# Kernel optimization log

Measured on AMD Instinct MI355X. Metric: run time of the kernel, lower is better.

## Reference

```python
import jax, jax.numpy as jnp
import numpy as np

DIM = 1024
NUM_HEADS = 16
HEAD_DIM = DIM // NUM_HEADS
B, L = 2, 2048


def setup_inputs() -> dict:
    key = jax.random.key(0)
    k_x, k_qkv, k_pw, k_pb = jax.random.split(key, 4)
    x = jax.random.normal(k_x, (B, L, DIM), dtype=jnp.float32)
    # nn.Linear(dim, 3*dim, bias=False): weight [3*dim, dim]; y = x @ W.T
    w_qkv = jax.random.normal(k_qkv, (3 * DIM, DIM), dtype=jnp.float32) * (DIM ** -0.5)
    # nn.Linear(dim, dim) with bias
    w_proj = jax.random.normal(k_pw, (DIM, DIM), dtype=jnp.float32) * (DIM ** -0.5)
    b_proj = jax.random.normal(k_pb, (DIM,), dtype=jnp.float32) * 0.01
    return {"x": x, "w_qkv": w_qkv, "w_proj": w_proj, "b_proj": b_proj}


def reference(x, w_qkv, w_proj, b_proj):
    Bx, Lx, C = x.shape
    qkv = x @ w_qkv.T  # [B, L, 3C]
    qkv = qkv.reshape(Bx, Lx, 3, NUM_HEADS, HEAD_DIM)
    q = jnp.transpose(qkv[:, :, 0], (0, 2, 1, 3))  # [B, H, L, D]
    k = jnp.transpose(qkv[:, :, 1], (0, 2, 1, 3))
    v = jnp.transpose(qkv[:, :, 2], (0, 2, 1, 3))
    attn = jnp.einsum('bhqd,bhkd->bhqk', q, k) * (HEAD_DIM ** -0.5)
    attn = jax.nn.softmax(attn, axis=-1)
    out = jnp.einsum('bhqk,bhkd->bhqd', attn, v)  # [B, H, L, D]
    out = jnp.transpose(out, (0, 2, 1, 3)).reshape(Bx, Lx, C)
    return out @ w_proj.T + b_proj
```

## Files before the change

### kernel.cpp

```cpp
#include <hip/hip_runtime.h>

#define DIM 1024
#define NH 16
#define HD 64
#define BB 2
#define LL 2048
#define BL (BB*LL)
#define NQKV (3*DIM)

typedef __bf16 bf16;
typedef __bf16 bf16x4 __attribute__((ext_vector_type(4)));
typedef __bf16 bf16x8 __attribute__((ext_vector_type(8)));
typedef float  f32x4  __attribute__((ext_vector_type(4)));

#define QSCALE 0.1803368801111204f

typedef __attribute__((address_space(3))) unsigned int lds_u32;
typedef __attribute__((address_space(1))) unsigned int glb_u32;

__device__ __forceinline__ void gld_lds16(const bf16* g, bf16* l) {
    __builtin_amdgcn_global_load_lds((const glb_u32*)g, (lds_u32*)l, 16, 0, 0);
}

#define C0 (BL*DIM/4)
#define C1 (NQKV*DIM/4)
#define C2 (DIM*DIM/4)
__global__ __launch_bounds__(256) void cvt_all(const float* __restrict__ x,
        const float* __restrict__ wq, const float* __restrict__ wp,
        bf16* __restrict__ xb, bf16* __restrict__ wqb, bf16* __restrict__ wpb) {
    int i = blockIdx.x * 256 + threadIdx.x;
    const float* in; bf16* out; int j;
    if (i < C0)            { in = x;  out = xb;  j = i; }
    else if (i < C0 + C1)  { in = wq; out = wqb; j = i - C0; }
    else                   { in = wp; out = wpb; j = i - C0 - C1; }
    float4 f = ((const float4*)in)[j];
    bf16x4 o = { (bf16)f.x, (bf16)f.y, (bf16)f.z, (bf16)f.w };
    ((bf16x4*)out)[j] = o;
}

__global__ __launch_bounds__(256, 3) void gemm_qkv(
        const bf16* __restrict__ A, const bf16* __restrict__ W,
        bf16* __restrict__ Qb, bf16* __restrict__ Kb, bf16* __restrict__ VTb) {
    __shared__ bf16 As[128][64];
    __shared__ bf16 Bs[128][64];
    const int tid = threadIdx.x;
    const int w = tid >> 6, lane = tid & 63, quad = lane >> 4, l16 = lane & 15;
    const int n0 = blockIdx.x * 128, m0 = blockIdx.y * 128;
    const int wm = (w & 1) * 64, wn = (w >> 1) * 64;
    f32x4 acc[4][4] = {};
    for (int k0 = 0; k0 < DIM; k0 += 64) {
        #pragma unroll
        for (int i = 0; i < 4; ++i) {
            int cb = w * 256 + i * 64;
            int gc = cb + lane;
            int r = gc >> 3;
            int cs = (gc & 7) ^ (r & 7);
            gld_lds16(A + (size_t)(m0 + r) * DIM + k0 + cs*8, &As[0][0] + cb * 8);
            gld_lds16(W + (size_t)(n0 + r) * DIM + k0 + cs*8, &Bs[0][0] + cb * 8);
        }
        __syncthreads();
        #pragma unroll
        for (int kc = 0; kc < 2; ++kc) {
            bf16x8 af[4], bfr[4];
            #pragma unroll
            for (int t = 0; t < 4; ++t) {
                int rw = wn + t*16 + l16;
                int cw = (kc*4 + quad) ^ (rw & 7);
                af[t] = *(const bf16x8*)(&Bs[0][0] + rw*64 + cw*8);
                int rx = wm + t*16 + l16;
                int cx = (kc*4 + quad) ^ (rx & 7);
                bfr[t] = *(const bf16x8*)(&As[0][0] + rx*64 + cx*8);
            }
            #pragma unroll
            for (int tm = 0; tm < 4; ++tm)
                #pragma unroll
                for (int tn = 0; tn < 4; ++tn)
                    acc[tm][tn] = __builtin_amdgcn_mfma_f32_16x16x32_bf16(
                                      af[tm], bfr[tn], acc[tm][tn], 0, 0, 0);
        }
        __syncthreads();
    }
    const int which = n0 >> 10;
    #pragma unroll
    for (int tm = 0; tm < 4; ++tm) {
        int nb = n0 + wn + tm*16 + quad*4;
        int rem = nb & 1023, h = rem >> 6, db = rem & 63;
        #pragma unroll
        for (int tn = 0; tn < 4; ++tn) {
            int m = m0 + wm + tn*16 + l16;
            int b = m >> 11, l = m & 2047, bh = (b << 4) | h;
            if (which == 0) {
                bf16x4 q4 = { (bf16)(acc[tm][tn][0] * QSCALE),
                              (bf16)(acc[tm][tn][1] * QSCALE),
                              (bf16)(acc[tm][tn][2] * QSCALE),
                              (bf16)(acc[tm][tn][3] * QSCALE) };
                *(bf16x4*)(Qb + ((size_t)bh << 17) + ((size_t)l << 6) + db) = q4;
            } else if (which == 1) {
                bf16x4 k4 = { (bf16)acc[tm][tn][0], (bf16)acc[tm][tn][1],
                              (bf16)acc[tm][tn][2], (bf16)acc[tm][tn][3] };
                *(bf16x4*)(Kb + ((size_t)bh << 17) + ((size_t)l << 6) + db) = k4;
            } else {
                #pragma unroll
                for (int r = 0; r < 4; ++r)
                    VTb[((size_t)bh << 17) + ((size_t)(db + r) << 11) + l] =
                        (bf16)acc[tm][tn][r];
            }
        }
    }
}

__global__ __launch_bounds__(256, 3) void gemm_proj(
        const bf16* __restrict__ A, const bf16* __restrict__ W,
        const float* __restrict__ bias, float* __restrict__ out) {
    __shared__ bf16 As[128][64];
    __shared__ bf16 Bs[64][64];
    const int tid = threadIdx.x;
    const int w = tid >> 6, lane = tid & 63, quad = lane >> 4, l16 = lane & 15;
    const int n0 = blockIdx.x * 64, m0 = blockIdx.y * 128;
    const int wm = (w & 1) * 64, wn = (w >> 1) * 32;
    f32x4 acc[2][4] = {};
    for (int k0 = 0; k0 < DIM; k0 += 64) {
        #pragma unroll
        for (int i = 0; i < 4; ++i) {
            int cb = w * 256 + i * 64;
            int gc = cb + lane;
            int r = gc >> 3;
            int cs = (gc & 7) ^ (r & 7);
            gld_lds16(A + (size_t)(m0 + r) * DIM + k0 + cs*8, &As[0][0] + cb * 8);
        }
        #pragma unroll
        for (int i = 0; i < 2; ++i) {
            int cb = w * 128 + i * 64;
            int gc = cb + lane;
            int r = gc >> 3;
            int cs = (gc & 7) ^ (r & 7);
            gld_lds16(W + (size_t)(n0 + r) * DIM + k0 + cs*8, &Bs[0][0] + cb * 8);
        }
        __syncthreads();
        #pragma unroll
        for (int kc = 0; kc < 2; ++kc) {
            bf16x8 af[2], bfr[4];
            #pragma unroll
            for (int t = 0; t < 2; ++t) {
                int rw = wn + t*16 + l16;
                int cw = (kc*4 + quad) ^ (rw & 7);
                af[t] = *(const bf16x8*)(&Bs[0][0] + rw*64 + cw*8);
            }
            #pragma unroll
            for (int t = 0; t < 4; ++t) {
                int rx = wm + t*16 + l16;
                int cx = (kc*4 + quad) ^ (rx & 7);
                bfr[t] = *(const bf16x8*)(&As[0][0] + rx*64 + cx*8);
            }
            #pragma unroll
            for (int tm = 0; tm < 2; ++tm)
                #pragma unroll
                for (int tn = 0; tn < 4; ++tn)
                    acc[tm][tn] = __builtin_amdgcn_mfma_f32_16x16x32_bf16(
                                      af[tm], bfr[tn], acc[tm][tn], 0, 0, 0);
        }
        __syncthreads();
    }
    #pragma unroll
    for (int tm = 0; tm < 2; ++tm) {
        int nb = n0 + wn + tm*16 + quad*4;
        float4 b4 = *(const float4*)&bias[nb];
        #pragma unroll
        for (int tn = 0; tn < 4; ++tn) {
            int m = m0 + wm + tn*16 + l16;
            float4 o4 = { acc[tm][tn][0] + b4.x, acc[tm][tn][1] + b4.y,
                          acc[tm][tn][2] + b4.z, acc[tm][tn][3] + b4.w };
            *(float4*)(out + (size_t)m * DIM + nb) = o4;
        }
    }
}

__global__ __launch_bounds__(256, 2) void attn(
        const bf16* __restrict__ Qb, const bf16* __restrict__ Kb,
        const bf16* __restrict__ VTb, bf16* __restrict__ AO) {
    __shared__ bf16 Ks[2][64][64];
    __shared__ bf16 VTs[2][64][64];
    const int tid = threadIdx.x;
    const int w = tid >> 6, lane = tid & 63, quad = lane >> 4, l16 = lane & 15;
    const int qt = blockIdx.x, bh = blockIdx.y;
    const bf16* Qg = Qb + ((size_t)bh << 17) + (size_t)(qt * 128) * 64;
    const bf16* Kg = Kb + ((size_t)bh << 17);
    const bf16* Vg = VTb + ((size_t)bh << 17);

    bf16x8 aq[2][2];
    #pragma unroll
    for (int sub = 0; sub < 2; ++sub)
        #pragma unroll
        for (int kd = 0; kd < 2; ++kd)
            aq[sub][kd] = *(const bf16x8*)(Qg + (size_t)(w*32 + sub*16 + l16) * 64
                                           + kd*32 + quad*8);

    bf16x8 onesf = {};
    if (l16 == 0)
        #pragma unroll
        for (int j = 0; j < 8; ++j) onesf[j] = (bf16)1.0f;

    f32x4 oacc[2][4] = {};
    f32x4 lacc[2] = {};
    bf16x8 apA[2][2], apB[2][2];

    auto stageK = [&](int kt, int buf) {
        #pragma unroll
        for (int i = 0; i < 2; ++i) {
            int gc = w*128 + i*64 + lane;
            int r = gc >> 3;
            int cs = (gc & 7) ^ (r & 7) ^ ((r >> 3) & 7) ^ ((r & 1) << 2);
            gld_lds16(Kg + (size_t)(kt*64 + r) * 64 + cs*8,
                      &Ks[buf][0][0] + gc * 8);
        }
    };
    auto stageV = [&](int kt, int buf) {
        #pragma unroll
        for (int i = 0; i < 2; ++i) {
            int gc = w*128 + i*64 + lane;
            int r = gc >> 3;
            int cs = (gc & 7) ^ (r & 7) ^ ((r >> 3) & 7);
            gld_lds16(Vg + (size_t)r * 2048 + kt*64 + cs*8,
                      &VTs[buf][0][0] + gc * 8);
        }
    };
    auto pv = [&](int pbuf, bf16x8 (&ap)[2][2]) {
        #pragma unroll
        for (int kk = 0; kk < 2; ++kk) {
            #pragma unroll
            for (int nt = 0; nt < 4; ++nt) {
                int row = nt*16 + l16;
                int cp = (kk*4 + quad) ^ (row & 7) ^ ((row >> 3) & 7);
                bf16x8 bv = *(const bf16x8*)(&VTs[pbuf][0][0] + row*64 + cp*8);
                #pragma unroll
                for (int sub = 0; sub < 2; ++sub)
                    oacc[sub][nt] = __builtin_amdgcn_mfma_f32_16x16x32_bf16(
                                        ap[sub][kk], bv, oacc[sub][nt], 0, 0, 0);
            }
            #pragma unroll
            for (int sub = 0; sub < 2; ++sub)
                lacc[sub] = __builtin_amdgcn_mfma_f32_16x16x32_bf16(
                                ap[sub][kk], onesf, lacc[sub], 0, 0, 0);
        }
    };

    auto body = [&](int kt, int cur, bf16x8 (&apw)[2][2], bf16x8 (&apr)[2][2]) {
        __syncthreads();
        if (kt < 31) stageK(kt + 1, cur ^ 1);
        stageV(kt, cur);

        f32x4 s[2][2][2] = {};
        #pragma unroll
        for (int kk = 0; kk < 2; ++kk)
            #pragma unroll
            for (int u = 0; u < 2; ++u)
                #pragma unroll
                for (int kd = 0; kd < 2; ++kd) {
                    int rk = kk*32 + ((l16 >> 2) << 3) + u*4 + (l16 & 3);
                    int cs = (kd*4 + quad) ^ (rk & 7) ^ ((rk >> 3) & 7)
                             ^ ((rk & 1) << 2);
                    bf16x8 ak = *(const bf16x8*)(&Ks[cur][0][0] + rk*64 + cs*8);
                    #pragma unroll
                    for (int sub = 0; sub < 2; ++sub)
                        s[sub][kk][u] = __builtin_amdgcn_mfma_f32_16x16x32_bf16(
                                            ak, aq[sub][kd], s[sub][kk][u], 0, 0, 0);
                }

        if (kt > 0) pv(cur ^ 1, apr);

        #pragma unroll
        for (int sub = 0; sub < 2; ++sub)
            #pragma unroll
            for (int kk = 0; kk < 2; ++kk) {
                bf16x8 p;
                #pragma unroll
                for (int u = 0; u < 2; ++u)
                    #pragma unroll
                    for (int r = 0; r < 4; ++r)
                        p[u*4 + r] = (bf16)exp2f(s[sub][kk][u][r]);
                apw[sub][kk] = p;
            }
    };

    stageK(0, 0);
    for (int kt2 = 0; kt2 < 32; kt2 += 2) {
        body(kt2,     0, apA, apB);
        body(kt2 + 1, 1, apB, apA);
    }
    __syncthreads();
    pv(1, apB);

    const int b = bh >> 4, h = bh & 15;
    #pragma unroll
    for (int sub = 0; sub < 2; ++sub)
        #pragma unroll
        for (int r = 0; r < 4; ++r) {
            float l = __shfl(lacc[sub][r], quad * 16, 64);
            float inv = 1.0f / l;
            int lq = qt*128 + w*32 + sub*16 + quad*4 + r;
            size_t rowbase = ((size_t)(b * 2048 + lq)) * DIM + h * 64;
            #pragma unroll
            for (int nt = 0; nt < 4; ++nt)
                AO[rowbase + nt*16 + l16] = (bf16)(oacc[sub][nt][r] * inv);
        }
}

extern "C" void kernel_launch(void* const* d_in, const int* in_sizes, int n_in,
                              void* d_out, int out_size, void* d_ws, size_t ws_size,
                              hipStream_t stream) {
    const float* x      = (const float*)d_in[0];
    const float* w_qkv  = (const float*)d_in[1];
    const float* w_proj = (const float*)d_in[2];
    const float* b_proj = (const float*)d_in[3];
    float* out = (float*)d_out;
    char* ws = (char*)d_ws;

    bf16* xb  = (bf16*)(ws);
    bf16* wqb = (bf16*)(ws + ( 8u << 20));
    bf16* wpb = (bf16*)(ws + (14u << 20));
    bf16* Qb  = (bf16*)(ws + (16u << 20));
    bf16* Kb  = (bf16*)(ws + (24u << 20));
    bf16* VTb = (bf16*)(ws + (32u << 20));
    bf16* AOb = (bf16*)(ws + (40u << 20));

    cvt_all<<<(C0 + C1 + C2) / 256, 256, 0, stream>>>(x, w_qkv, w_proj, xb, wqb, wpb);
    gemm_qkv<<<dim3(NQKV/128, BL/128), 256, 0, stream>>>(xb, wqb, Qb, Kb, VTb);
    attn<<<dim3(LL/128, BB*NH),        256, 0, stream>>>(Qb, Kb, VTb, AOb);
    gemm_proj<<<dim3(DIM/64, BL/128),  256, 0, stream>>>(AOb, wpb, b_proj, out);
}
```

Baseline: 186.8 us.

## Load K/V fragments directly from global into registers, drop LDS staging

The attention kernel stops staging K and V^T tiles through double-buffered LDS with global_load_lds and barriers. Each wave now loads its MFMA operand fragments straight from global memory into registers, software-pipelined so the next K/V loads are issued around the PV and S MFMAs. Block indices are also remapped with an XOR-free swizzle so consecutive blocks cover different heads, which changes L2 locality. This removes __syncthreads and LDS traffic, but each of the four waves now fetches the same K/V data separately, multiplying global/L2 reads and register pressure.

```diff
diff --git a/kernel.cpp b/kernel.cpp
--- a/kernel.cpp
+++ b/kernel.cpp
@@ -178,11 +178,11 @@
 __global__ __launch_bounds__(256, 2) void attn(
         const bf16* __restrict__ Qb, const bf16* __restrict__ Kb,
         const bf16* __restrict__ VTb, bf16* __restrict__ AO) {
-    __shared__ bf16 Ks[2][64][64];
-    __shared__ bf16 VTs[2][64][64];
     const int tid = threadIdx.x;
     const int w = tid >> 6, lane = tid & 63, quad = lane >> 4, l16 = lane & 15;
-    const int qt = blockIdx.x, bh = blockIdx.y;
+    const int linear = blockIdx.y * 16 + blockIdx.x;
+    const int swz = (linear & 7) * 64 + (linear >> 3);
+    const int qt = swz & 15, bh = swz >> 4;
     const bf16* Qg = Qb + ((size_t)bh << 17) + (size_t)(qt * 128) * 64;
     const bf16* Kg = Kb + ((size_t)bh << 17);
     const bf16* Vg = VTb + ((size_t)bh << 17);
@@ -200,74 +200,63 @@
         #pragma unroll
         for (int j = 0; j < 8; ++j) onesf[j] = (bf16)1.0f;
 
+    int kofs[2][2][2];
+    #pragma unroll
+    for (int kk = 0; kk < 2; ++kk)
+        #pragma unroll
+        for (int u = 0; u < 2; ++u)
+            #pragma unroll
+            for (int kd = 0; kd < 2; ++kd) {
+                int rk = kk*32 + ((l16 >> 2) << 3) + u*4 + (l16 & 3);
+                kofs[kk][u][kd] = rk*64 + kd*32 + quad*8;
+            }
+    int vofs[2][4];
+    #pragma unroll
+    for (int kk = 0; kk < 2; ++kk)
+        #pragma unroll
+        for (int nt = 0; nt < 4; ++nt)
+            vofs[kk][nt] = (nt*16 + l16) * 2048 + kk*32 + quad*8;
+
     f32x4 oacc[2][4] = {};
     f32x4 lacc[2] = {};
-    bf16x8 apA[2][2], apB[2][2];
-
-    auto stageK = [&](int kt, int buf) {
-        #pragma unroll
-        for (int i = 0; i < 2; ++i) {
-            int gc = w*128 + i*64 + lane;
-            int r = gc >> 3;
-            int cs = (gc & 7) ^ (r & 7) ^ ((r >> 3) & 7) ^ ((r & 1) << 2);
-            gld_lds16(Kg + (size_t)(kt*64 + r) * 64 + cs*8,
-                      &Ks[buf][0][0] + gc * 8);
-        }
+    const f32x4 zero4 = {};
+    bf16x8 ap[2][2];
+    bf16x8 kf[2][2][2];
+    bf16x8 vf[2][4];
+
+    auto loadK = [&](int kt) {
+        const int kb = kt * 4096;
+        #pragma unroll
+        for (int kk = 0; kk < 2; ++kk)
+            #pragma unroll
+            for (int u = 0; u < 2; ++u)
+                #pragma unroll
+                for (int kd = 0; kd < 2; ++kd)
+                    kf[kk][u][kd] =
+                        *(const bf16x8*)(Kg + kb + kofs[kk][u][kd]);
     };
-    auto stageV = [&](int kt, int buf) {
-        #pragma unroll
-        for (int i = 0; i < 2; ++i) {
-            int gc = w*128 + i*64 + lane;
-            int r = gc >> 3;
-            int cs = (gc & 7) ^ (r & 7) ^ ((r >> 3) & 7);
-            gld_lds16(Vg + (size_t)r * 2048 + kt*64 + cs*8,
-                      &VTs[buf][0][0] + gc * 8);
-        }
+    auto loadV = [&](int kt) {
+        const int vb = kt * 64;
+        #pragma unroll
+        for (int kk = 0; kk < 2; ++kk)
+            #pragma unroll
+            for (int nt = 0; nt < 4; ++nt)
+                vf[kk][nt] = *(const bf16x8*)(Vg + vb + vofs[kk][nt]);
     };
-    auto pv = [&](int pbuf, bf16x8 (&ap)[2][2]) {
-        #pragma unroll
-        for (int kk = 0; kk < 2; ++kk) {
-            #pragma unroll
-            for (int nt = 0; nt < 4; ++nt) {
-                int row = nt*16 + l16;
-                int cp = (kk*4 + quad) ^ (row & 7) ^ ((row >> 3) & 7);
-                bf16x8 bv = *(const bf16x8*)(&VTs[pbuf][0][0] + row*64 + cp*8);
-                #pragma unroll
-                for (int sub = 0; sub < 2; ++sub)
-                    oacc[sub][nt] = __builtin_amdgcn_mfma_f32_16x16x32_bf16(
-                                        ap[sub][kk], bv, oacc[sub][nt], 0, 0, 0);
-            }
-            #pragma unroll
-            for (int sub = 0; sub < 2; ++sub)
-                lacc[sub] = __builtin_amdgcn_mfma_f32_16x16x32_bf16(
-                                ap[sub][kk], onesf, lacc[sub], 0, 0, 0);
-        }
-    };
-
-    auto body = [&](int kt, int cur, bf16x8 (&apw)[2][2], bf16x8 (&apr)[2][2]) {
-        __syncthreads();
-        if (kt < 31) stageK(kt + 1, cur ^ 1);
-        stageV(kt, cur);
-
-        f32x4 s[2][2][2] = {};
+    auto sphase = [&]() {
+        f32x4 s[2][2][2];
         #pragma unroll
         for (int kk = 0; kk < 2; ++kk)
             #pragma unroll
             for (int u = 0; u < 2; ++u)
                 #pragma unroll
-                for (int kd = 0; kd < 2; ++kd) {
-                    int rk = kk*32 + ((l16 >> 2) << 3) + u*4 + (l16 & 3);
-                    int cs = (kd*4 + quad) ^ (rk & 7) ^ ((rk >> 3) & 7)
-                             ^ ((rk & 1) << 2);
-                    bf16x8 ak = *(const bf16x8*)(&Ks[cur][0][0] + rk*64 + cs*8);
-                    #pragma unroll
-                    for (int sub = 0; sub < 2; ++sub)
-                        s[sub][kk][u] = __builtin_amdgcn_mfma_f32_16x16x32_bf16(
-                                            ak, aq[sub][kd], s[sub][kk][u], 0, 0, 0);
+                for (int sub = 0; sub < 2; ++sub) {
+                    s[sub][kk][u] = __builtin_amdgcn_mfma_f32_16x16x32_bf16(
+                                        kf[kk][u][0], aq[sub][0], zero4, 0, 0, 0);
+                    s[sub][kk][u] = __builtin_amdgcn_mfma_f32_16x16x32_bf16(
+                                        kf[kk][u][1], aq[sub][1], s[sub][kk][u],
+                                        0, 0, 0);
                 }
-
-        if (kt > 0) pv(cur ^ 1, apr);
-
         #pragma unroll
         for (int sub = 0; sub < 2; ++sub)
             #pragma unroll
@@ -278,17 +267,36 @@
                     #pragma unroll
                     for (int r = 0; r < 4; ++r)
                         p[u*4 + r] = (bf16)exp2f(s[sub][kk][u][r]);
-                apw[sub][kk] = p;
+                ap[sub][kk] = p;
             }
     };
-
-    stageK(0, 0);
-    for (int kt2 = 0; kt2 < 32; kt2 += 2) {
-        body(kt2,     0, apA, apB);
-        body(kt2 + 1, 1, apB, apA);
-    }
-    __syncthreads();
-    pv(1, apB);
+    auto pv = [&]() {
+        #pragma unroll
+        for (int kk = 0; kk < 2; ++kk) {
+            #pragma unroll
+            for (int nt = 0; nt < 4; ++nt)
+                #pragma unroll
+                for (int sub = 0; sub < 2; ++sub)
+                    oacc[sub][nt] = __builtin_amdgcn_mfma_f32_16x16x32_bf16(
+                                        ap[sub][kk], vf[kk][nt], oacc[sub][nt],
+                                        0, 0, 0);
+            #pragma unroll
+            for (int sub = 0; sub < 2; ++sub)
+                lacc[sub] = __builtin_amdgcn_mfma_f32_16x16x32_bf16(
+                                ap[sub][kk], onesf, lacc[sub], 0, 0, 0);
+        }
+    };
+
+    loadK(0);
+    loadV(0);
+    sphase();
+    for (int kt = 1; kt < 32; ++kt) {
+        loadK(kt);
+        pv();
+        loadV(kt);
+        sphase();
+    }
+    pv();
 
     const int b = bh >> 4, h = bh & 15;
     #pragma unroll
```

Result: slower. 244.9 us (+31.1%).

## Split KV tile across wave halves in attention with 512-thread blocks and LDS reduction

Applied to the files above, without the earlier changes.

The attention kernel now uses 512-thread blocks covering 256 query rows. Each group of four waves takes one half of every 64-key tile, and the two halves' partial outputs and row sums are combined through shared memory at the end. The change also swizzles the block-to-(q-tile, head) mapping and moves the PV step ahead of the QK step within each iteration. The aim is more K/V reuse per LDS load and better use of the matrix units, at the cost of more registers per wave, a final LDS reduction, and fewer blocks in the grid.

```diff
diff --git a/kernel.cpp b/kernel.cpp
--- a/kernel.cpp
+++ b/kernel.cpp
@@ -175,24 +175,28 @@
     }
 }
 
-__global__ __launch_bounds__(256, 2) void attn(
+__global__ __launch_bounds__(512, 2) void attn(
         const bf16* __restrict__ Qb, const bf16* __restrict__ Kb,
         const bf16* __restrict__ VTb, bf16* __restrict__ AO) {
-    __shared__ bf16 Ks[2][64][64];
-    __shared__ bf16 VTs[2][64][64];
+    __shared__ __align__(16) char smem[33280];
+    bf16* KsP  = (bf16*)smem;
+    bf16* VTsP = KsP + 8192;
     const int tid = threadIdx.x;
     const int w = tid >> 6, lane = tid & 63, quad = lane >> 4, l16 = lane & 15;
-    const int qt = blockIdx.x, bh = blockIdx.y;
-    const bf16* Qg = Qb + ((size_t)bh << 17) + (size_t)(qt * 128) * 64;
+    const int qw = w & 3, kvh = w >> 2;
+    const int linear = blockIdx.y * 8 + blockIdx.x;
+    const int swz = (linear & 7) * 32 + (linear >> 3);
+    const int qt = swz & 7, bh = swz >> 3;
+    const bf16* Qg = Qb + ((size_t)bh << 17) + (size_t)(qt * 256) * 64;
     const bf16* Kg = Kb + ((size_t)bh << 17);
     const bf16* Vg = VTb + ((size_t)bh << 17);
 
-    bf16x8 aq[2][2];
+    bf16x8 aq[4][2];
     #pragma unroll
-    for (int sub = 0; sub < 2; ++sub)
+    for (int sub = 0; sub < 4; ++sub)
         #pragma unroll
         for (int kd = 0; kd < 2; ++kd)
-            aq[sub][kd] = *(const bf16x8*)(Qg + (size_t)(w*32 + sub*16 + l16) * 64
+            aq[sub][kd] = *(const bf16x8*)(Qg + (size_t)(qw*64 + sub*16 + l16) * 64
                                            + kd*32 + quad*8);
 
     bf16x8 onesf = {};
@@ -200,109 +204,136 @@
         #pragma unroll
         for (int j = 0; j < 8; ++j) onesf[j] = (bf16)1.0f;
 
-    f32x4 oacc[2][4] = {};
-    f32x4 lacc[2] = {};
-    bf16x8 apA[2][2], apB[2][2];
+    f32x4 oacc[4][4] = {};
+    f32x4 lacc[4] = {};
+    const f32x4 zero4 = {};
+    bf16x8 ap[4];
 
     auto stageK = [&](int kt, int buf) {
-        #pragma unroll
-        for (int i = 0; i < 2; ++i) {
-            int gc = w*128 + i*64 + lane;
-            int r = gc >> 3;
-            int cs = (gc & 7) ^ (r & 7) ^ ((r >> 3) & 7) ^ ((r & 1) << 2);
-            gld_lds16(Kg + (size_t)(kt*64 + r) * 64 + cs*8,
-                      &Ks[buf][0][0] + gc * 8);
-        }
+        int r = tid >> 3;
+        int cs = (tid & 7) ^ (r & 7) ^ ((r >> 3) & 7) ^ ((r & 1) << 2);
+        gld_lds16(Kg + (size_t)(kt*64 + r) * 64 + cs*8, KsP + buf*4096 + tid*8);
     };
     auto stageV = [&](int kt, int buf) {
-        #pragma unroll
-        for (int i = 0; i < 2; ++i) {
-            int gc = w*128 + i*64 + lane;
-            int r = gc >> 3;
-            int cs = (gc & 7) ^ (r & 7) ^ ((r >> 3) & 7);
-            gld_lds16(Vg + (size_t)r * 2048 + kt*64 + cs*8,
-                      &VTs[buf][0][0] + gc * 8);
-        }
+        int r = tid >> 3;
+        int cs = (tid & 7) ^ (r & 7) ^ ((r >> 3) & 7);
+        gld_lds16(Vg + (size_t)r * 2048 + kt*64 + cs*8, VTsP + buf*4096 + tid*8);
     };
-    auto pv = [&](int pbuf, bf16x8 (&ap)[2][2]) {
-        #pragma unroll
-        for (int kk = 0; kk < 2; ++kk) {
-            #pragma unroll
-            for (int nt = 0; nt < 4; ++nt) {
-                int row = nt*16 + l16;
-                int cp = (kk*4 + quad) ^ (row & 7) ^ ((row >> 3) & 7);
-                bf16x8 bv = *(const bf16x8*)(&VTs[pbuf][0][0] + row*64 + cp*8);
-                #pragma unroll
-                for (int sub = 0; sub < 2; ++sub)
-                    oacc[sub][nt] = __builtin_amdgcn_mfma_f32_16x16x32_bf16(
-                                        ap[sub][kk], bv, oacc[sub][nt], 0, 0, 0);
-            }
-            #pragma unroll
-            for (int sub = 0; sub < 2; ++sub)
-                lacc[sub] = __builtin_amdgcn_mfma_f32_16x16x32_bf16(
-                                ap[sub][kk], onesf, lacc[sub], 0, 0, 0);
-        }
+    auto pv = [&](int pbuf) {
+        #pragma unroll
+        for (int nt = 0; nt < 4; ++nt) {
+            int row = nt*16 + l16;
+            int cp = (kvh*4 + quad) ^ (row & 7) ^ ((row >> 3) & 7);
+            bf16x8 bv = *(const bf16x8*)(VTsP + pbuf*4096 + row*64 + cp*8);
+            #pragma unroll
+            for (int sub = 0; sub < 4; ++sub)
+                oacc[sub][nt] = __builtin_amdgcn_mfma_f32_16x16x32_bf16(
+                                    ap[sub], bv, oacc[sub][nt], 0, 0, 0);
+        }
+        #pragma unroll
+        for (int sub = 0; sub < 4; ++sub)
+            lacc[sub] = __builtin_amdgcn_mfma_f32_16x16x32_bf16(
+                            ap[sub], onesf, lacc[sub], 0, 0, 0);
     };
 
-    auto body = [&](int kt, int cur, bf16x8 (&apw)[2][2], bf16x8 (&apr)[2][2]) {
+    auto body = [&](int kt, int cur) {
         __syncthreads();
         if (kt < 31) stageK(kt + 1, cur ^ 1);
         stageV(kt, cur);
 
-        f32x4 s[2][2][2] = {};
-        #pragma unroll
-        for (int kk = 0; kk < 2; ++kk)
+        if (kt > 0) pv(cur ^ 1);
+
+        f32x4 s[4][2];
+        #pragma unroll
+        for (int u = 0; u < 2; ++u) {
+            bf16x8 kf0, kf1;
+            int rk = kvh*32 + ((l16 >> 2) << 3) + u*4 + (l16 & 3);
+            int f = (rk & 7) ^ ((rk >> 3) & 7) ^ ((rk & 1) << 2);
+            kf0 = *(const bf16x8*)(KsP + cur*4096 + rk*64 + ((0*4 + quad) ^ f)*8);
+            kf1 = *(const bf16x8*)(KsP + cur*4096 + rk*64 + ((1*4 + quad) ^ f)*8);
+            #pragma unroll
+            for (int sub = 0; sub < 4; ++sub) {
+                s[sub][u] = __builtin_amdgcn_mfma_f32_16x16x32_bf16(
+                                kf0, aq[sub][0], zero4, 0, 0, 0);
+                s[sub][u] = __builtin_amdgcn_mfma_f32_16x16x32_bf16(
+                                kf1, aq[sub][1], s[sub][u], 0, 0, 0);
+            }
+        }
+
+        #pragma unroll
+        for (int sub = 0; sub < 4; ++sub) {
+            bf16x8 p;
             #pragma unroll
             for (int u = 0; u < 2; ++u)
                 #pragma unroll
-                for (int kd = 0; kd < 2; ++kd) {
-                    int rk = kk*32 + ((l16 >> 2) << 3) + u*4 + (l16 & 3);
-                    int cs = (kd*4 + quad) ^ (rk & 7) ^ ((rk >> 3) & 7)
-                             ^ ((rk & 1) << 2);
-                    bf16x8 ak = *(const bf16x8*)(&Ks[cur][0][0] + rk*64 + cs*8);
-                    #pragma unroll
-                    for (int sub = 0; sub < 2; ++sub)
-                        s[sub][kk][u] = __builtin_amdgcn_mfma_f32_16x16x32_bf16(
-                                            ak, aq[sub][kd], s[sub][kk][u], 0, 0, 0);
-                }
-
-        if (kt > 0) pv(cur ^ 1, apr);
-
-        #pragma unroll
-        for (int sub = 0; sub < 2; ++sub)
-            #pragma unroll
-            for (int kk = 0; kk < 2; ++kk) {
-                bf16x8 p;
-                #pragma unroll
-                for (int u = 0; u < 2; ++u)
-                    #pragma unroll
-                    for (int r = 0; r < 4; ++r)
-                        p[u*4 + r] = (bf16)exp2f(s[sub][kk][u][r]);
-                apw[sub][kk] = p;
-            }
+                for (int r = 0; r < 4; ++r)
+                    p[u*4 + r] = (bf16)exp2f(s[sub][u][r]);
+            ap[sub] = p;
+        }
     };
 
     stageK(0, 0);
     for (int kt2 = 0; kt2 < 32; kt2 += 2) {
-        body(kt2,     0, apA, apB);
-        body(kt2 + 1, 1, apB, apA);
+        body(kt2,     0);
+        body(kt2 + 1, 1);
     }
     __syncthreads();
-    pv(1, apB);
-
+    pv(1);
+
+    float* OredF = (float*)smem;
+    float* LredF = (float*)(smem + 32768);
     const int b = bh >> 4, h = bh & 15;
     #pragma unroll
-    for (int sub = 0; sub < 2; ++sub)
-        #pragma unroll
-        for (int r = 0; r < 4; ++r) {
-            float l = __shfl(lacc[sub][r], quad * 16, 64);
-            float inv = 1.0f / l;
-            int lq = qt*128 + w*32 + sub*16 + quad*4 + r;
-            size_t rowbase = ((size_t)(b * 2048 + lq)) * DIM + h * 64;
-            #pragma unroll
-            for (int nt = 0; nt < 4; ++nt)
-                AO[rowbase + nt*16 + l16] = (bf16)(oacc[sub][nt][r] * inv);
-        }
+    for (int t = 0; t < 2; ++t) {
+        __syncthreads();
+        if (kvh == 1 && (qw >> 1) == t) {
+            int slot = qw & 1;
+            #pragma unroll
+            for (int sub = 0; sub < 4; ++sub)
+                #pragma unroll
+                for (int nt = 0; nt < 4; ++nt)
+                    #pragma unroll
+                    for (int r = 0; r < 4; ++r)
+                        OredF[((slot*4 + sub)*16 + quad*4 + r)*64 + nt*16 + l16]
+                            = oacc[sub][nt][r];
+            if (l16 == 0)
+                #pragma unroll
+                for (int sub = 0; sub < 4; ++sub)
+                    #pragma unroll
+                    for (int r = 0; r < 4; ++r)
+                        LredF[(slot*4 + sub)*16 + quad*4 + r] = lacc[sub][r];
+        }
+        __syncthreads();
+        if (kvh == 0 && (qw >> 1) == t) {
+            int slot = qw & 1;
+            #pragma unroll
+            for (int sub = 0; sub < 4; ++sub)
+                #pragma unroll
+                for (int nt = 0; nt < 4; ++nt)
+                    #pragma unroll
+                    for (int r = 0; r < 4; ++r)
+                        oacc[sub][nt][r] +=
+                            OredF[((slot*4 + sub)*16 + quad*4 + r)*64 + nt*16 + l16];
+            if (l16 == 0)
+                #pragma unroll
+                for (int sub = 0; sub < 4; ++sub)
+                    #pragma unroll
+                    for (int r = 0; r < 4; ++r)
+                        lacc[sub][r] += LredF[(slot*4 + sub)*16 + quad*4 + r];
+            #pragma unroll
+            for (int sub = 0; sub < 4; ++sub)
+                #pragma unroll
+                for (int r = 0; r < 4; ++r) {
+                    float l = __shfl(lacc[sub][r], quad * 16, 64);
+                    float inv = 1.0f / l;
+                    int lq = qt*256 + qw*64 + sub*16 + quad*4 + r;
+                    size_t rowbase = ((size_t)(b * 2048 + lq)) * DIM + h * 64;
+                    #pragma unroll
+                    for (int nt = 0; nt < 4; ++nt)
+                        AO[rowbase + nt*16 + l16] = (bf16)(oacc[sub][nt][r] * inv);
+                }
+        }
+    }
 }
 
 extern "C" void kernel_launch(void* const* d_in, const int* in_sizes, int n_in,
@@ -325,6 +356,6 @@
 
     cvt_all<<<(C0 + C1 + C2) / 256, 256, 0, stream>>>(x, w_qkv, w_proj, xb, wqb, wpb);
     gemm_qkv<<<dim3(NQKV/128, BL/128), 256, 0, stream>>>(xb, wqb, Qb, Kb, VTb);
-    attn<<<dim3(LL/128, BB*NH),        256, 0, stream>>>(Qb, Kb, VTb, AOb);
+    attn<<<dim3(LL/256, BB*NH),        512, 0, stream>>>(Qb, Kb, VTb, AOb);
     gemm_proj<<<dim3(DIM/64, BL/128),  256, 0, stream>>>(AOb, wpb, b_proj, out);
 }
```

After: 181.5 us. 1.03x faster.
